# Optimization experiments

Measured on AMD Instinct MI355X. Metric: run time of the kernel, lower is better.

The kernel has to match this reference:

```python
import math
import jax, jax.numpy as jnp
import numpy as np

B, T, D = 8, 2048, 512
EPS = 1e-5


def _gate(x, W, b, a, g, beta):
    # Linear -> PReLU (single shared slope a) -> LayerNorm -> sigmoid
    h = x @ W.T + b
    h = jnp.where(h >= 0, h, a * h)
    mu = jnp.mean(h, axis=-1, keepdims=True)
    var = jnp.var(h, axis=-1, keepdims=True)
    h = (h - mu) / jnp.sqrt(var + EPS) * g + beta
    return jax.nn.sigmoid(h)


def setup_inputs() -> dict:
    key = jax.random.key(0)
    ks = jax.random.split(key, 12)
    lin = lambda k: jax.random.normal(k, (D, D), jnp.float32) * 0.02
    z = jnp.zeros((D,), jnp.float32)
    o = jnp.ones((D,), jnp.float32)
    a0 = jnp.float32(0.25)  # PReLU default init
    inp = {
        "query": jax.random.normal(ks[0], (B, T, D), jnp.float32),
        "value": jax.random.normal(ks[1], (B, T, D), jnp.float32),
        "aux_emb": jax.random.normal(ks[2], (B, 1, D), jnp.float32),
        # ragged valid lengths in [T//2, T] to keep every sample realistic
        "input_len": jax.random.randint(ks[3], (B,), T // 2, T + 1),
        "Wq": lin(ks[4]), "bq": z,
        "Wqg": lin(ks[5]), "bqg": z, "aq": a0, "gq": o, "betaq": z,
        "Wkg": lin(ks[6]), "bkg": z, "ak": a0, "gk": o, "betak": z,
        "Wvg": lin(ks[7]), "bvg": z, "av": a0, "gv": o, "betav": z,
        "Wsig": lin(ks[8]), "bsig": z,
        "Wtan": lin(ks[9]), "btan": z,
    }
    return inp


def reference(query, value, aux_emb, input_len,
              Wq, bq,
              Wqg, bqg, aq, gq, betaq,
              Wkg, bkg, ak, gk, betak,
              Wvg, bvg, av, gv, betav,
              Wsig, bsig, Wtan, btan):
    q = query @ Wq.T + bq
    q = q * _gate(aux_emb, Wqg, bqg, aq, gq, betaq)          # [B,T,D]
    k = value * _gate(aux_emb, Wkg, bkg, ak, gk, betak)      # [B,T,D]
    vg = _gate(aux_emb, Wvg, bvg, av, gv, betav)             # [B,1,D]
    vg = jax.nn.sigmoid(vg @ Wsig.T + bsig) * jnp.tanh(vg @ Wtan.T + btan)
    v = value * vg                                           # [B,T,D]

    w = jnp.einsum('btd,bsd->bts', q, k) / math.sqrt(D)      # [B,T,T]
    r = jnp.arange(T)
    causal = (r[:, None] >= r[None, :]).astype(w.dtype)      # tril ones
    w = w * causal
    w = jnp.where(w == 0.0, -jnp.inf, w)  # torch quirk: exact zeros -> -inf
    L = input_len[:, None, None]                              # [B,1,1]
    invalid = (r[None, :, None] < L) & (r[None, None, :] >= L)
    w = jnp.where(invalid, -jnp.inf, w)
    p = jax.nn.softmax(w, axis=-1)
    # rows beyond input_len are padding: zero them (torch code produced NaN
    # there via -inf*0; intended semantics is zeroed padding rows)
    row_valid = (r[None, :, None] < L).astype(p.dtype)        # [B,T,1]
    p = p * row_valid
    return p @ v                                              # [B,T,D]
```

## Files before the change

kernel.cpp:

```cpp
#include <hip/hip_runtime.h>
#include <hip/hip_bf16.h>
#include <stdint.h>

#define BB 8
#define TT 2048
#define DD 512

typedef __attribute__((ext_vector_type(8))) __bf16 bf16x8;
typedef __attribute__((ext_vector_type(4))) float f32x4;

__device__ __forceinline__ unsigned short f2bf(float f) {
    unsigned u = __builtin_bit_cast(unsigned, f);
    unsigned r = u + 0x7fffu + ((u >> 16) & 1u);
    return (unsigned short)(r >> 16);
}

__device__ __forceinline__ void gload_lds16(const unsigned short* g, unsigned short* l) {
    __builtin_amdgcn_global_load_lds(
        (const __attribute__((address_space(1))) void*)g,
        (__attribute__((address_space(3))) void*)l, 16, 0, 0);
}

__global__ __launch_bounds__(256) void gates_mv1(
    const float* __restrict__ aux,
    const float* __restrict__ Wqg, const float* __restrict__ bqg, const float* __restrict__ aq,
    const float* __restrict__ Wkg, const float* __restrict__ bkg, const float* __restrict__ ak,
    const float* __restrict__ Wvg, const float* __restrict__ bvg, const float* __restrict__ av,
    float* __restrict__ h) {
    __shared__ float saux[BB * DD];
    int tid = threadIdx.x;
#pragma unroll
    for (int i = 0; i < 4; i++) {
        int idx = tid + i * 256;
        ((float4*)saux)[idx] = ((const float4*)aux)[idx];
    }
    __syncthreads();
    int wave = (blockIdx.x * 256 + tid) >> 6;
    int lane = tid & 63;
    int g = wave >> 9, r = wave & 511;
    const float* W    = (g == 0) ? Wqg : (g == 1) ? Wkg : Wvg;
    const float* bias = (g == 0) ? bqg : (g == 1) ? bkg : bvg;
    const float* alpha = (g == 0) ? aq : (g == 1) ? ak : av;
    const float4* Wrow = (const float4*)(W + (size_t)r * DD);
    float acc[BB];
#pragma unroll
    for (int b = 0; b < BB; b++) acc[b] = 0.f;
#pragma unroll
    for (int c = 0; c < 2; c++) {
        float4 w4 = Wrow[lane + c * 64];
#pragma unroll
        for (int b = 0; b < BB; b++) {
            float4 a4 = ((const float4*)(saux + b * DD))[lane + c * 64];
            acc[b] += w4.x * a4.x + w4.y * a4.y + w4.z * a4.z + w4.w * a4.w;
        }
    }
#pragma unroll
    for (int b = 0; b < BB; b++) {
#pragma unroll
        for (int s = 1; s < 64; s <<= 1) acc[b] += __shfl_xor(acc[b], s, 64);
    }
    if (lane == 0) {
        float bi = bias[r], a = alpha[0];
#pragma unroll
        for (int b = 0; b < BB; b++) {
            float v = acc[b] + bi;
            v = (v >= 0.f) ? v : a * v;
            h[(g * BB + b) * DD + r] = v;
        }
    }
}

__global__ __launch_bounds__(512) void gates_norm(
    const float* __restrict__ h,
    const float* __restrict__ gq, const float* __restrict__ betaq,
    const float* __restrict__ gk, const float* __restrict__ betak,
    const float* __restrict__ gv, const float* __restrict__ betav,
    float* __restrict__ qgate, float* __restrict__ kgate, float* __restrict__ vg) {
    int g = blockIdx.x >> 3, b = blockIdx.x & 7, tid = threadIdx.x;
    __shared__ float red[DD], red2[DD];
    float hv = h[(g * BB + b) * DD + tid];
    red[tid] = hv; red2[tid] = hv * hv;
    __syncthreads();
    for (int s = 256; s > 0; s >>= 1) {
        if (tid < s) { red[tid] += red[tid + s]; red2[tid] += red2[tid + s]; }
        __syncthreads();
    }
    float mu = red[0] * (1.f / DD);
    float var = red2[0] * (1.f / DD) - mu * mu;
    const float* gg = (g == 0) ? gq : (g == 1) ? gk : gv;
    const float* be = (g == 0) ? betaq : (g == 1) ? betak : betav;
    float val = (hv - mu) * rsqrtf(var + 1e-5f) * gg[tid] + be[tid];
    float sg = 1.f / (1.f + expf(-val));
    float* outp = (g == 0) ? qgate : (g == 1) ? kgate : vg;
    outp[b * DD + tid] = sg;
}

__global__ __launch_bounds__(256) void gates_mv2(
    const float* __restrict__ vg,
    const float* __restrict__ Wsig, const float* __restrict__ bsig,
    const float* __restrict__ Wtan, const float* __restrict__ btan,
    float* __restrict__ vgate) {
    __shared__ float svg[BB * DD];
    int tid = threadIdx.x;
#pragma unroll
    for (int i = 0; i < 4; i++) {
        int idx = tid + i * 256;
        ((float4*)svg)[idx] = ((const float4*)vg)[idx];
    }
    __syncthreads();
    int r = (blockIdx.x * 256 + tid) >> 6;
    int lane = tid & 63;
    const float4* Ws = (const float4*)(Wsig + (size_t)r * DD);
    const float4* Wt = (const float4*)(Wtan + (size_t)r * DD);
    float as_[BB], at_[BB];
#pragma unroll
    for (int b = 0; b < BB; b++) { as_[b] = 0.f; at_[b] = 0.f; }
#pragma unroll
    for (int c = 0; c < 2; c++) {
        float4 w1 = Ws[lane + c * 64];
        float4 w2 = Wt[lane + c * 64];
#pragma unroll
        for (int b = 0; b < BB; b++) {
            float4 a4 = ((const float4*)(svg + b * DD))[lane + c * 64];
            as_[b] += w1.x * a4.x + w1.y * a4.y + w1.z * a4.z + w1.w * a4.w;
            at_[b] += w2.x * a4.x + w2.y * a4.y + w2.z * a4.z + w2.w * a4.w;
        }
    }
#pragma unroll
    for (int b = 0; b < BB; b++) {
#pragma unroll
        for (int s = 1; s < 64; s <<= 1) {
            as_[b] += __shfl_xor(as_[b], s, 64);
            at_[b] += __shfl_xor(at_[b], s, 64);
        }
    }
    if (lane == 0) {
        float b1 = bsig[r], b2 = btan[r];
#pragma unroll
        for (int b = 0; b < BB; b++) {
            float s1 = 1.f / (1.f + expf(-(as_[b] + b1)));
            float s2 = tanhf(at_[b] + b2);
            vgate[b * DD + r] = s1 * s2;
        }
    }
}

__global__ __launch_bounds__(256) void convert_kernel(
    const float* __restrict__ query, const float* __restrict__ Wq,
    const float* __restrict__ value,
    const float* __restrict__ kgate, const float* __restrict__ vgate,
    unsigned short* __restrict__ queryb, unsigned short* __restrict__ Wqb,
    unsigned short* __restrict__ kb, unsigned short* __restrict__ vbT) {
    __shared__ float tile[32][33];
    int bi = blockIdx.x, tid = threadIdx.x;
    if (bi < 8192) {
        int idx = bi * 256 + tid;
        float4 q4 = ((const float4*)query)[idx];
        ushort4 oq;
        oq.x = f2bf(q4.x); oq.y = f2bf(q4.y); oq.z = f2bf(q4.z); oq.w = f2bf(q4.w);
        ((ushort4*)queryb)[idx] = oq;
    } else if (bi < 8448) {
        int idx = (bi - 8192) * 256 + tid;
        float4 w4 = ((const float4*)Wq)[idx];
        ushort4 o;
        o.x = f2bf(w4.x); o.y = f2bf(w4.y); o.z = f2bf(w4.z); o.w = f2bf(w4.w);
        ((ushort4*)Wqb)[idx] = o;
    } else {
        int vb = bi - 8448;
        int tIdx = vb & 63, dIdx = (vb >> 6) & 15, b = vb >> 10;
        int t0 = tIdx * 32, d0 = dIdx * 32;
        int tx = tid & 31, ty = tid >> 5;
        float kg = kgate[b * DD + d0 + tx];
#pragma unroll
        for (int i = 0; i < 4; i++) {
            int t = t0 + ty + i * 8;
            float v = value[((size_t)b * TT + t) * DD + d0 + tx];
            tile[ty + i * 8][tx] = v;
            kb[((size_t)b * TT + t) * DD + d0 + tx] = f2bf(v * kg);
        }
        __syncthreads();
#pragma unroll
        for (int i = 0; i < 4; i++) {
            int d = d0 + ty + i * 8;
            float g = vgate[b * DD + d];
            vbT[((size_t)b * DD + d) * TT + t0 + tx] = f2bf(tile[tx][ty + i * 8] * g);
        }
    }
}

#define STAGE_AB(BUF, K0)                                                                 \
    _Pragma("unroll") for (int i = 0; i < 2; i++) {                                       \
        int idx = tid * 8 + i * 2048;                                                     \
        int r = idx >> 5;                                                                 \
        int cg = ((idx >> 3) & 3) ^ ((r >> 1) & 3);                                       \
        gload_lds16(&Ap_[(size_t)r * lda_ + (K0) + cg * 8], &As[BUF][idx]);               \
        gload_lds16(&Bp_[(size_t)r * ldb_ + (K0) + cg * 8], &Bs[BUF][idx]);               \
    }

#define GEMM_CORE(APTR, ALDA, BPTR, BLDA, KSTART, KEND)                                   \
    __shared__ __align__(16) unsigned short As[2][128 * 32];                              \
    __shared__ __align__(16) unsigned short Bs[2][128 * 32];                              \
    const unsigned short* Ap_ = (APTR);                                                   \
    const unsigned short* Bp_ = (BPTR);                                                   \
    const int lda_ = (ALDA), ldb_ = (BLDA);                                               \
    int tid = threadIdx.x;                                                                \
    int lane = tid & 63, wid = tid >> 6;                                                  \
    int wm = (wid >> 1) * 64, wn = (wid & 1) * 64;                                        \
    int lm = lane & 15, quad = lane >> 4;                                                 \
    f32x4 acc[4][4];                                                                      \
    _Pragma("unroll") for (int im = 0; im < 4; im++)                                      \
        _Pragma("unroll") for (int in = 0; in < 4; in++)                                  \
            acc[im][in] = (f32x4){0.f, 0.f, 0.f, 0.f};                                    \
    STAGE_AB(0, (KSTART))                                                                 \
    int cur_ = 0;                                                                         \
    for (int k0 = (KSTART); k0 < (KEND); k0 += 32) {                                      \
        __syncthreads();                                                                  \
        if (k0 + 32 < (KEND)) { STAGE_AB(cur_ ^ 1, k0 + 32) }                             \
        bf16x8 af[4], bf_[4];                                                             \
        _Pragma("unroll") for (int i = 0; i < 4; i++) {                                   \
            int row = wm + i * 16 + lm;                                                   \
            af[i] = *(const bf16x8*)&As[cur_][row * 32 + (quad ^ ((row >> 1) & 3)) * 8];  \
        }                                                                                 \
        _Pragma("unroll") for (int i = 0; i < 4; i++) {                                   \
            int row = wn + i * 16 + lm;                                                   \
            bf_[i] = *(const bf16x8*)&Bs[cur_][row * 32 + (quad ^ ((row >> 1) & 3)) * 8]; \
        }                                                                                 \
        _Pragma("unroll") for (int im = 0; im < 4; im++)                                  \
            _Pragma("unroll") for (int in = 0; in < 4; in++)                              \
                acc[im][in] = __builtin_amdgcn_mfma_f32_16x16x32_bf16(af[im], bf_[in],    \
                                                                     acc[im][in], 0, 0, 0);\
        cur_ ^= 1;                                                                        \
    }

__global__ __launch_bounds__(256) void qgemm_kernel(
    const unsigned short* __restrict__ Amat, const unsigned short* __restrict__ Bmat,
    const float* __restrict__ bq, const float* __restrict__ qgate,
    unsigned short* __restrict__ qb) {
    int m0 = blockIdx.x * 128, n0 = blockIdx.y * 128;
    const unsigned short* Ap = Amat + (size_t)m0 * DD;
    const unsigned short* Bp = Bmat + (size_t)n0 * DD;
    GEMM_CORE(Ap, DD, Bp, DD, 0, DD)
    int b = m0 >> 11;
#pragma unroll
    for (int im = 0; im < 4; im++) {
        int row = m0 + wm + im * 16 + quad * 4;
#pragma unroll
        for (int in = 0; in < 4; in++) {
            int col = n0 + wn + in * 16 + lm;
            float bias = bq[col];
            float g = qgate[b * DD + col];
#pragma unroll
            for (int r = 0; r < 4; r++) {
                float v = (acc[im][in][r] + bias) * g;
                qb[(size_t)(row + r) * DD + col] = f2bf(v);
            }
        }
    }
}

__global__ __launch_bounds__(256) void scores_kernel(
    const unsigned short* __restrict__ qb, const unsigned short* __restrict__ kb,
    unsigned short* __restrict__ P, float* __restrict__ rowsum) {
    int b = blockIdx.z;
    int idx = blockIdx.x;
    int mt = (int)((sqrtf(8.f * idx + 1.f) - 1.f) * 0.5f);
    while ((mt + 1) * (mt + 2) / 2 <= idx) mt++;
    while (mt * (mt + 1) / 2 > idx) mt--;
    int nt = idx - mt * (mt + 1) / 2;
    int t0 = mt * 128, s0 = nt * 128;
    const unsigned short* Ap = qb + ((size_t)b * TT + t0) * DD;
    const unsigned short* Bp = kb + ((size_t)b * TT + s0) * DD;
    GEMM_CORE(Ap, DD, Bp, DD, 0, DD)
    const float scale = 0.044194173824159216f;
    unsigned short* Ptile = P + ((size_t)b * 136 + (size_t)mt * (mt + 1) / 2 + nt) * 16384;
#pragma unroll
    for (int im = 0; im < 4; im++) {
        int ltb = wm + im * 16 + quad * 4;
        float rs[4] = {0.f, 0.f, 0.f, 0.f};
#pragma unroll
        for (int in = 0; in < 4; in++) {
            int ls = wn + in * 16 + lm;
            int s = s0 + ls;
#pragma unroll
            for (int r = 0; r < 4; r++) {
                float p = (s <= t0 + ltb + r) ? expf(acc[im][in][r] * scale) : 0.f;
                Ptile[(size_t)(ltb + r) * 128 + ls] = f2bf(p);
                rs[r] += p;
            }
        }
#pragma unroll
        for (int r = 0; r < 4; r++) {
            float v = rs[r];
            v += __shfl_xor(v, 1, 64);
            v += __shfl_xor(v, 2, 64);
            v += __shfl_xor(v, 4, 64);
            v += __shfl_xor(v, 8, 64);
            if (lm == 0) atomicAdd(&rowsum[b * TT + t0 + ltb + r], v);
        }
    }
}

__global__ __launch_bounds__(256) void out_kernel(
    const unsigned short* __restrict__ P, const unsigned short* __restrict__ vbT,
    const float* __restrict__ rowsum, const int* __restrict__ input_len,
    float* __restrict__ out) {
    int nt = blockIdx.x;
    int pr = blockIdx.y;
    int b = blockIdx.z;
    int n0 = nt * 128;
    int L = input_len[b];

    __shared__ __align__(16) unsigned short As[2][64 * 64];
    __shared__ __align__(16) unsigned short Bs[2][128 * 64];
    int tid = threadIdx.x;
    int lane = tid & 63, wid = tid >> 6;
    int wm = (wid >> 1) * 32, wn = (wid & 1) * 64;
    int lm = lane & 15, quad = lane >> 4;

#pragma unroll
    for (int half = 0; half < 2; half++) {
        int mt = half ? (31 - pr) : pr;
        int t0 = mt * 64;
        int mt128 = mt >> 1;
        int rowoff = (mt & 1) * 64;
        size_t triBase = ((size_t)b * 136 + (size_t)mt128 * (mt128 + 1) / 2) * 16384;
        int ksteps = mt + 1;

        f32x4 acc[2][4];
#pragma unroll
        for (int im = 0; im < 2; im++)
#pragma unroll
            for (int in = 0; in < 4; in++) acc[im][in] = (f32x4){0.f, 0.f, 0.f, 0.f};

#define OUT_STAGE(BUF, KS)                                                              \
        {                                                                               \
            int k0s = (KS) * 64;                                                        \
            int stile = k0s >> 7;                                                       \
            int coloff = k0s & 64;                                                      \
            _Pragma("unroll") for (int i = 0; i < 2; i++) {                             \
                int idx = tid * 8 + i * 2048;                                           \
                int r = idx >> 6;                                                       \
                int c = (idx >> 3) & 7;                                                 \
                int cs = c ^ (r & 7);                                                   \
                const unsigned short* ag = P + triBase + (size_t)stile * 16384 +        \
                                           (size_t)(rowoff + r) * 128 + coloff + cs * 8;\
                gload_lds16(ag, &As[BUF][idx]);                                         \
            }                                                                           \
            _Pragma("unroll") for (int i = 0; i < 4; i++) {                             \
                int idx = tid * 8 + i * 2048;                                           \
                int r = idx >> 6;                                                       \
                int c = (idx >> 3) & 7;                                                 \
                int cs = c ^ (r & 7);                                                   \
                gload_lds16(&vbT[(size_t)(b * DD + n0 + r) * TT + k0s + cs * 8],        \
                            &Bs[BUF][idx]);                                             \
            }                                                                           \
        }

        OUT_STAGE(0, 0)
        int cur = 0;
        for (int ks = 0; ks < ksteps; ks++) {
            __syncthreads();
            if (ks + 1 < ksteps) { OUT_STAGE(cur ^ 1, ks + 1) }
            bf16x8 af[2][2], bf_[4][2];
#pragma unroll
            for (int kk = 0; kk < 2; kk++) {
#pragma unroll
                for (int i = 0; i < 2; i++) {
                    int row = wm + i * 16 + lm;
                    af[i][kk] = *(const bf16x8*)&As[cur][row * 64 + ((kk * 4 + quad) ^ (row & 7)) * 8];
                }
#pragma unroll
                for (int i = 0; i < 4; i++) {
                    int row = wn + i * 16 + lm;
                    bf_[i][kk] = *(const bf16x8*)&Bs[cur][row * 64 + ((kk * 4 + quad) ^ (row & 7)) * 8];
                }
            }
#pragma unroll
            for (int kk = 0; kk < 2; kk++)
#pragma unroll
                for (int im = 0; im < 2; im++)
#pragma unroll
                    for (int in = 0; in < 4; in++)
                        acc[im][in] = __builtin_amdgcn_mfma_f32_16x16x32_bf16(
                            af[im][kk], bf_[in][kk], acc[im][in], 0, 0, 0);
            cur ^= 1;
        }
        __syncthreads();
#undef OUT_STAGE

#pragma unroll
        for (int im = 0; im < 2; im++) {
            int tbase = t0 + wm + im * 16 + quad * 4;
#pragma unroll
            for (int r = 0; r < 4; r++) {
                int t = tbase + r;
                float inv = 1.f / rowsum[b * TT + t];
                bool valid = (t < L);
#pragma unroll
                for (int in = 0; in < 4; in++) {
                    int n = n0 + wn + in * 16 + lm;
                    float o = valid ? acc[im][in][r] * inv : 0.f;
                    out[((size_t)b * TT + t) * DD + n] = o;
                }
            }
        }
    }
}

extern "C" void kernel_launch(void* const* d_in, const int* in_sizes, int n_in,
                              void* d_out, int out_size, void* d_ws, size_t ws_size,
                              hipStream_t stream) {
    const float* query = (const float*)d_in[0];
    const float* value = (const float*)d_in[1];
    const float* aux   = (const float*)d_in[2];
    const int*   ilen  = (const int*)d_in[3];
    const float* Wq    = (const float*)d_in[4];
    const float* bq    = (const float*)d_in[5];
    const float* Wqg   = (const float*)d_in[6];
    const float* bqg   = (const float*)d_in[7];
    const float* aq    = (const float*)d_in[8];
    const float* gq    = (const float*)d_in[9];
    const float* betaq = (const float*)d_in[10];
    const float* Wkg   = (const float*)d_in[11];
    const float* bkg   = (const float*)d_in[12];
    const float* ak    = (const float*)d_in[13];
    const float* gk    = (const float*)d_in[14];
    const float* betak = (const float*)d_in[15];
    const float* Wvg   = (const float*)d_in[16];
    const float* bvg   = (const float*)d_in[17];
    const float* av    = (const float*)d_in[18];
    const float* gv    = (const float*)d_in[19];
    const float* betav = (const float*)d_in[20];
    const float* Wsig  = (const float*)d_in[21];
    const float* bsig  = (const float*)d_in[22];
    const float* Wtan  = (const float*)d_in[23];
    const float* btan  = (const float*)d_in[24];

    char* ws = (char*)d_ws;
    float* qgate          = (float*)(ws + 0);
    float* kgate          = (float*)(ws + 16384);
    float* vgate          = (float*)(ws + 32768);
    float* rowsum         = (float*)(ws + 49152);
    unsigned short* Wqb   = (unsigned short*)(ws + 114688);
    unsigned short* queryb= (unsigned short*)(ws + 638976);
    unsigned short* qb    = (unsigned short*)(ws + 17416192);
    unsigned short* kb    = (unsigned short*)(ws + 34193408);
    unsigned short* vbT   = (unsigned short*)(ws + 50970624);
    unsigned short* P     = (unsigned short*)(ws + 67747840);
    float* hbuf           = (float*)(ws + 67747840);
    float* vg             = (float*)(ws + 67747840 + 49152);

    hipMemsetAsync(rowsum, 0, BB * TT * sizeof(float), stream);

    gates_mv1<<<384, 256, 0, stream>>>(aux, Wqg, bqg, aq, Wkg, bkg, ak, Wvg, bvg, av, hbuf);
    gates_norm<<<24, 512, 0, stream>>>(hbuf, gq, betaq, gk, betak, gv, betav,
                                       qgate, kgate, vg);
    gates_mv2<<<128, 256, 0, stream>>>(vg, Wsig, bsig, Wtan, btan, vgate);

    convert_kernel<<<16640, 256, 0, stream>>>(query, Wq, value, kgate, vgate,
                                              queryb, Wqb, kb, vbT);
    qgemm_kernel<<<dim3((BB * TT) / 128, DD / 128), 256, 0, stream>>>(queryb, Wqb, bq, qgate, qb);
    scores_kernel<<<dim3(136, 1, BB), 256, 0, stream>>>(qb, kb, P, rowsum);
    out_kernel<<<dim3(4, 16, BB), 256, 0, stream>>>(P, vbT, rowsum, ilen, (float*)d_out);
}
```

Before: 273.2 us.

## Fuse scores and PV into one flash-style attention kernel without materialized P

Replaces the separate scores kernel (which wrote bf16 exp-scores to a global P buffer plus atomic rowsums) and the output GEMM kernel with a single attention kernel. Each 512-thread block processes two paired 32-row query strips, keeping Q in LDS, streaming K and V tiles through a shared double buffer, writing P only to LDS and accumulating row sums locally. This removes the global P round trip, the rowsum memset and one kernel launch. In exchange there are only 256 blocks, each with small 32-row tiles and many barriers, and K/V are re-read once per strip, so occupancy and reuse may be lower.

```diff
diff --git a/kernel.cpp b/kernel.cpp
--- a/kernel.cpp
+++ b/kernel.cpp
@@ -258,153 +258,187 @@
     }
 }
 
-__global__ __launch_bounds__(256) void scores_kernel(
+__global__ __launch_bounds__(512) void attn_kernel(
     const unsigned short* __restrict__ qb, const unsigned short* __restrict__ kb,
-    unsigned short* __restrict__ P, float* __restrict__ rowsum) {
-    int b = blockIdx.z;
-    int idx = blockIdx.x;
-    int mt = (int)((sqrtf(8.f * idx + 1.f) - 1.f) * 0.5f);
-    while ((mt + 1) * (mt + 2) / 2 <= idx) mt++;
-    while (mt * (mt + 1) / 2 > idx) mt--;
-    int nt = idx - mt * (mt + 1) / 2;
-    int t0 = mt * 128, s0 = nt * 128;
-    const unsigned short* Ap = qb + ((size_t)b * TT + t0) * DD;
-    const unsigned short* Bp = kb + ((size_t)b * TT + s0) * DD;
-    GEMM_CORE(Ap, DD, Bp, DD, 0, DD)
+    const unsigned short* __restrict__ vbT, const int* __restrict__ input_len,
+    float* __restrict__ out) {
+    int bid = blockIdx.x;
+    int p = bid >> 3, b = bid & 7;
+    int L = input_len[b];
+    int tid = threadIdx.x;
+    int lane = tid & 63, w = tid >> 6;
+    int lm = lane & 15, quad = lane >> 4;
+    const size_t bTT = (size_t)b * TT;
     const float scale = 0.044194173824159216f;
-    unsigned short* Ptile = P + ((size_t)b * 136 + (size_t)mt * (mt + 1) / 2 + nt) * 16384;
-#pragma unroll
-    for (int im = 0; im < 4; im++) {
-        int ltb = wm + im * 16 + quad * 4;
-        float rs[4] = {0.f, 0.f, 0.f, 0.f};
-#pragma unroll
-        for (int in = 0; in < 4; in++) {
-            int ls = wn + in * 16 + lm;
-            int s = s0 + ls;
+
+    __shared__ __align__(16) unsigned short Qs[32 * 512];
+    __shared__ __align__(16) unsigned short KV[2][2048 * 8];
+    __shared__ __align__(16) unsigned short Ps[32 * 256];
+    __shared__ float rs_lds[32];
+
+#define STAGE_K(DST, KV0, D0)                                                     \
+    _Pragma("unroll") for (int i_ = 0; i_ < 4; i_++) {                            \
+        int idx_ = tid + i_ * 512;                                                \
+        int r_ = idx_ >> 3, c_ = idx_ & 7;                                        \
+        int g_ = c_ ^ (r_ & 7);                                                   \
+        gload_lds16(&kb[(bTT + (KV0) + r_) * DD + (D0) + g_ * 8],                 \
+                    &KV[DST][idx_ * 8]);                                          \
+    }
+#define STAGE_V(DST, KVC)                                                         \
+    _Pragma("unroll") for (int i_ = 0; i_ < 4; i_++) {                            \
+        int idx_ = tid + i_ * 512;                                                \
+        int r_ = idx_ >> 2, c_ = idx_ & 3;                                        \
+        int g_ = c_ ^ (r_ & 3);                                                   \
+        gload_lds16(&vbT[((size_t)(b * DD) + r_) * TT + (KVC) + g_ * 8],          \
+                    &KV[DST][idx_ * 8]);                                          \
+    }
+
+#pragma unroll 1
+    for (int half = 0; half < 2; half++) {
+        int strip = half ? (63 - p) : p;
+        int t0 = strip * 32;
+        int nk = (strip >> 3) + 1;
+
+        __syncthreads();
+#pragma unroll
+        for (int i_ = 0; i_ < 4; i_++) {
+            int idx_ = tid + i_ * 512;
+            int r_ = idx_ >> 6, c_ = idx_ & 63;
+            int gc_ = (c_ & 56) | ((c_ ^ r_) & 7);
+            gload_lds16(&qb[(bTT + t0 + r_) * DD + gc_ * 8], &Qs[idx_ * 8]);
+        }
+        STAGE_K(0, 0, 0)
+        int buf = 0;
+
+        f32x4 oacc[2][4];
+#pragma unroll
+        for (int mi = 0; mi < 2; mi++)
+#pragma unroll
+            for (int ni = 0; ni < 4; ni++) oacc[mi][ni] = (f32x4){0.f, 0.f, 0.f, 0.f};
+        float rsum[2][4];
+#pragma unroll
+        for (int mi = 0; mi < 2; mi++)
+#pragma unroll
+            for (int r = 0; r < 4; r++) rsum[mi][r] = 0.f;
+
+        for (int m = 0; m < nk; m++) {
+            int kv0 = m * 256;
+            f32x4 sacc[2][2];
+#pragma unroll
+            for (int mi = 0; mi < 2; mi++)
+#pragma unroll
+                for (int ni = 0; ni < 2; ni++) sacc[mi][ni] = (f32x4){0.f, 0.f, 0.f, 0.f};
+
+#pragma unroll 1
+            for (int ds = 0; ds < 8; ds++) {
+                __syncthreads();
+                if (ds < 7) { STAGE_K(buf ^ 1, kv0, (ds + 1) * 64) }
+                else        { STAGE_V(buf ^ 1, kv0) }
+#pragma unroll
+                for (int kk = 0; kk < 2; kk++) {
+                    bf16x8 aq[2], bk[2];
+#pragma unroll
+                    for (int mi = 0; mi < 2; mi++) {
+                        int row = mi * 16 + lm;
+                        int c = ds * 8 + kk * 4 + quad;
+                        int sc = (c & 56) | ((c ^ row) & 7);
+                        aq[mi] = *(const bf16x8*)&Qs[(row << 9) + sc * 8];
+                    }
+#pragma unroll
+                    for (int ni = 0; ni < 2; ni++) {
+                        int row = w * 32 + ni * 16 + lm;
+                        int sc = (kk * 4 + quad) ^ (row & 7);
+                        bk[ni] = *(const bf16x8*)&KV[buf][(row << 6) + sc * 8];
+                    }
+#pragma unroll
+                    for (int mi = 0; mi < 2; mi++)
+#pragma unroll
+                        for (int ni = 0; ni < 2; ni++)
+                            sacc[mi][ni] = __builtin_amdgcn_mfma_f32_16x16x32_bf16(
+                                aq[mi], bk[ni], sacc[mi][ni], 0, 0, 0);
+                }
+                buf ^= 1;
+            }
+
+#pragma unroll
+            for (int mi = 0; mi < 2; mi++)
+#pragma unroll
+                for (int ni = 0; ni < 2; ni++)
+#pragma unroll
+                    for (int r = 0; r < 4; r++) {
+                        int trow = mi * 16 + quad * 4 + r;
+                        int t = t0 + trow;
+                        int e = w * 32 + ni * 16 + lm;
+                        int s = kv0 + e;
+                        float pv = (s <= t) ? expf(sacc[mi][ni][r] * scale) : 0.f;
+                        rsum[mi][r] += pv;
+                        int c = e >> 3, o = e & 7;
+                        int sc = (c & 24) | ((c ^ trow) & 7);
+                        Ps[trow * 256 + sc * 8 + o] = f2bf(pv);
+                    }
+
+#pragma unroll 1
+            for (int kc = 0; kc < 8; kc++) {
+                __syncthreads();
+                if (kc < 7)           { STAGE_V(buf ^ 1, kv0 + (kc + 1) * 32) }
+                else if (m + 1 < nk)  { STAGE_K(buf ^ 1, kv0 + 256, 0) }
+                bf16x8 pa[2], vb[4];
+#pragma unroll
+                for (int mi = 0; mi < 2; mi++) {
+                    int row = mi * 16 + lm;
+                    int c = kc * 4 + quad;
+                    int sc = (c & 24) | ((c ^ row) & 7);
+                    pa[mi] = *(const bf16x8*)&Ps[row * 256 + sc * 8];
+                }
+#pragma unroll
+                for (int ni = 0; ni < 4; ni++) {
+                    int row = w * 64 + ni * 16 + lm;
+                    int sc = quad ^ (row & 3);
+                    vb[ni] = *(const bf16x8*)&KV[buf][(row << 5) + sc * 8];
+                }
+#pragma unroll
+                for (int mi = 0; mi < 2; mi++)
+#pragma unroll
+                    for (int ni = 0; ni < 4; ni++)
+                        oacc[mi][ni] = __builtin_amdgcn_mfma_f32_16x16x32_bf16(
+                            pa[mi], vb[ni], oacc[mi][ni], 0, 0, 0);
+                buf ^= 1;
+            }
+        }
+
+        __syncthreads();
+        if (tid < 32) rs_lds[tid] = 0.f;
+        __syncthreads();
+#pragma unroll
+        for (int mi = 0; mi < 2; mi++)
 #pragma unroll
             for (int r = 0; r < 4; r++) {
-                float p = (s <= t0 + ltb + r) ? expf(acc[im][in][r] * scale) : 0.f;
-                Ptile[(size_t)(ltb + r) * 128 + ls] = f2bf(p);
-                rs[r] += p;
+                float v = rsum[mi][r];
+                v += __shfl_xor(v, 1, 64);
+                v += __shfl_xor(v, 2, 64);
+                v += __shfl_xor(v, 4, 64);
+                v += __shfl_xor(v, 8, 64);
+                if (lm == 0) atomicAdd(&rs_lds[mi * 16 + quad * 4 + r], v);
             }
-        }
-#pragma unroll
-        for (int r = 0; r < 4; r++) {
-            float v = rs[r];
-            v += __shfl_xor(v, 1, 64);
-            v += __shfl_xor(v, 2, 64);
-            v += __shfl_xor(v, 4, 64);
-            v += __shfl_xor(v, 8, 64);
-            if (lm == 0) atomicAdd(&rowsum[b * TT + t0 + ltb + r], v);
-        }
-    }
-}
-
-__global__ __launch_bounds__(256) void out_kernel(
-    const unsigned short* __restrict__ P, const unsigned short* __restrict__ vbT,
-    const float* __restrict__ rowsum, const int* __restrict__ input_len,
-    float* __restrict__ out) {
-    int nt = blockIdx.x;
-    int pr = blockIdx.y;
-    int b = blockIdx.z;
-    int n0 = nt * 128;
-    int L = input_len[b];
-
-    __shared__ __align__(16) unsigned short As[2][64 * 64];
-    __shared__ __align__(16) unsigned short Bs[2][128 * 64];
-    int tid = threadIdx.x;
-    int lane = tid & 63, wid = tid >> 6;
-    int wm = (wid >> 1) * 32, wn = (wid & 1) * 64;
-    int lm = lane & 15, quad = lane >> 4;
-
-#pragma unroll
-    for (int half = 0; half < 2; half++) {
-        int mt = half ? (31 - pr) : pr;
-        int t0 = mt * 64;
-        int mt128 = mt >> 1;
-        int rowoff = (mt & 1) * 64;
-        size_t triBase = ((size_t)b * 136 + (size_t)mt128 * (mt128 + 1) / 2) * 16384;
-        int ksteps = mt + 1;
-
-        f32x4 acc[2][4];
-#pragma unroll
-        for (int im = 0; im < 2; im++)
-#pragma unroll
-            for (int in = 0; in < 4; in++) acc[im][in] = (f32x4){0.f, 0.f, 0.f, 0.f};
-
-#define OUT_STAGE(BUF, KS)                                                              \
-        {                                                                               \
-            int k0s = (KS) * 64;                                                        \
-            int stile = k0s >> 7;                                                       \
-            int coloff = k0s & 64;                                                      \
-            _Pragma("unroll") for (int i = 0; i < 2; i++) {                             \
-                int idx = tid * 8 + i * 2048;                                           \
-                int r = idx >> 6;                                                       \
-                int c = (idx >> 3) & 7;                                                 \
-                int cs = c ^ (r & 7);                                                   \
-                const unsigned short* ag = P + triBase + (size_t)stile * 16384 +        \
-                                           (size_t)(rowoff + r) * 128 + coloff + cs * 8;\
-                gload_lds16(ag, &As[BUF][idx]);                                         \
-            }                                                                           \
-            _Pragma("unroll") for (int i = 0; i < 4; i++) {                             \
-                int idx = tid * 8 + i * 2048;                                           \
-                int r = idx >> 6;                                                       \
-                int c = (idx >> 3) & 7;                                                 \
-                int cs = c ^ (r & 7);                                                   \
-                gload_lds16(&vbT[(size_t)(b * DD + n0 + r) * TT + k0s + cs * 8],        \
-                            &Bs[BUF][idx]);                                             \
-            }                                                                           \
-        }
-
-        OUT_STAGE(0, 0)
-        int cur = 0;
-        for (int ks = 0; ks < ksteps; ks++) {
-            __syncthreads();
-            if (ks + 1 < ksteps) { OUT_STAGE(cur ^ 1, ks + 1) }
-            bf16x8 af[2][2], bf_[4][2];
-#pragma unroll
-            for (int kk = 0; kk < 2; kk++) {
-#pragma unroll
-                for (int i = 0; i < 2; i++) {
-                    int row = wm + i * 16 + lm;
-                    af[i][kk] = *(const bf16x8*)&As[cur][row * 64 + ((kk * 4 + quad) ^ (row & 7)) * 8];
-                }
-#pragma unroll
-                for (int i = 0; i < 4; i++) {
-                    int row = wn + i * 16 + lm;
-                    bf_[i][kk] = *(const bf16x8*)&Bs[cur][row * 64 + ((kk * 4 + quad) ^ (row & 7)) * 8];
+        __syncthreads();
+#pragma unroll
+        for (int mi = 0; mi < 2; mi++)
+#pragma unroll
+            for (int r = 0; r < 4; r++) {
+                int trow = mi * 16 + quad * 4 + r;
+                int t = t0 + trow;
+                float inv = 1.f / rs_lds[trow];
+                bool valid = (t < L);
+#pragma unroll
+                for (int ni = 0; ni < 4; ni++) {
+                    int n = w * 64 + ni * 16 + lm;
+                    float o = valid ? oacc[mi][ni][r] * inv : 0.f;
+                    out[(bTT + t) * DD + n] = o;
                 }
             }
-#pragma unroll
-            for (int kk = 0; kk < 2; kk++)
-#pragma unroll
-                for (int im = 0; im < 2; im++)
-#pragma unroll
-                    for (int in = 0; in < 4; in++)
-                        acc[im][in] = __builtin_amdgcn_mfma_f32_16x16x32_bf16(
-                            af[im][kk], bf_[in][kk], acc[im][in], 0, 0, 0);
-            cur ^= 1;
-        }
-        __syncthreads();
-#undef OUT_STAGE
-
-#pragma unroll
-        for (int im = 0; im < 2; im++) {
-            int tbase = t0 + wm + im * 16 + quad * 4;
-#pragma unroll
-            for (int r = 0; r < 4; r++) {
-                int t = tbase + r;
-                float inv = 1.f / rowsum[b * TT + t];
-                bool valid = (t < L);
-#pragma unroll
-                for (int in = 0; in < 4; in++) {
-                    int n = n0 + wn + in * 16 + lm;
-                    float o = valid ? acc[im][in][r] * inv : 0.f;
-                    out[((size_t)b * TT + t) * DD + n] = o;
-                }
-            }
-        }
-    }
+    }
+#undef STAGE_K
+#undef STAGE_V
 }
 
 extern "C" void kernel_launch(void* const* d_in, const int* in_sizes, int n_in,
@@ -440,17 +474,13 @@
     float* qgate          = (float*)(ws + 0);
     float* kgate          = (float*)(ws + 16384);
     float* vgate          = (float*)(ws + 32768);
-    float* rowsum         = (float*)(ws + 49152);
     unsigned short* Wqb   = (unsigned short*)(ws + 114688);
     unsigned short* queryb= (unsigned short*)(ws + 638976);
     unsigned short* qb    = (unsigned short*)(ws + 17416192);
     unsigned short* kb    = (unsigned short*)(ws + 34193408);
     unsigned short* vbT   = (unsigned short*)(ws + 50970624);
-    unsigned short* P     = (unsigned short*)(ws + 67747840);
     float* hbuf           = (float*)(ws + 67747840);
     float* vg             = (float*)(ws + 67747840 + 49152);
-
-    hipMemsetAsync(rowsum, 0, BB * TT * sizeof(float), stream);
 
     gates_mv1<<<384, 256, 0, stream>>>(aux, Wqg, bqg, aq, Wkg, bkg, ak, Wvg, bvg, av, hbuf);
     gates_norm<<<24, 512, 0, stream>>>(hbuf, gq, betaq, gk, betak, gv, betav,
@@ -460,6 +490,5 @@
     convert_kernel<<<16640, 256, 0, stream>>>(query, Wq, value, kgate, vgate,
                                               queryb, Wqb, kb, vbT);
     qgemm_kernel<<<dim3((BB * TT) / 128, DD / 128), 256, 0, stream>>>(queryb, Wqb, bq, qgate, qb);
-    scores_kernel<<<dim3(136, 1, BB), 256, 0, stream>>>(qb, kb, P, rowsum);
-    out_kernel<<<dim3(4, 16, BB), 256, 0, stream>>>(P, vbT, rowsum, ilen, (float*)d_out);
-}
+    attn_kernel<<<256, 512, 0, stream>>>(qb, kb, vbT, ilen, (float*)d_out);
+}
```

Result: slower. 302.9 us (+10.9%).

## Vectorize value transpose/convert tiles and interleave batches across workgroup order

Applied to the files above, without the earlier changes.

The value conversion path moves from 32x32 tiles with scalar loads and stores to 64x64 tiles using float4 loads and 16-byte bf16 stores for both the gated key copy and the transposed value copy. This reduces the block count and the number of narrow memory transactions. The scores and output kernels also remap the block index so the batch index varies fastest, spreading each batch's work across the dispatch order. The transposed LDS read with a 65-float stride may still cause some bank conflicts.

```diff
diff --git a/kernel.cpp b/kernel.cpp
--- a/kernel.cpp
+++ b/kernel.cpp
@@ -8,6 +8,7 @@
 
 typedef __attribute__((ext_vector_type(8))) __bf16 bf16x8;
 typedef __attribute__((ext_vector_type(4))) float f32x4;
+typedef __attribute__((ext_vector_type(8))) unsigned short ushort8_t;
 
 __device__ __forceinline__ unsigned short f2bf(float f) {
     unsigned u = __builtin_bit_cast(unsigned, f);
@@ -151,7 +152,7 @@
     const float* __restrict__ kgate, const float* __restrict__ vgate,
     unsigned short* __restrict__ queryb, unsigned short* __restrict__ Wqb,
     unsigned short* __restrict__ kb, unsigned short* __restrict__ vbT) {
-    __shared__ float tile[32][33];
+    __shared__ float tileF[64][65];
     int bi = blockIdx.x, tid = threadIdx.x;
     if (bi < 8192) {
         int idx = bi * 256 + tid;
@@ -167,24 +168,42 @@
         ((ushort4*)Wqb)[idx] = o;
     } else {
         int vb = bi - 8448;
-        int tIdx = vb & 63, dIdx = (vb >> 6) & 15, b = vb >> 10;
-        int t0 = tIdx * 32, d0 = dIdx * 32;
-        int tx = tid & 31, ty = tid >> 5;
-        float kg = kgate[b * DD + d0 + tx];
-#pragma unroll
-        for (int i = 0; i < 4; i++) {
-            int t = t0 + ty + i * 8;
-            float v = value[((size_t)b * TT + t) * DD + d0 + tx];
-            tile[ty + i * 8][tx] = v;
-            kb[((size_t)b * TT + t) * DD + d0 + tx] = f2bf(v * kg);
-        }
+        int tIdx = vb & 31, dIdx = (vb >> 5) & 7, b = vb >> 8;
+        int t0 = tIdx * 64, d0 = dIdx * 64;
+        int row = tid >> 2;
+        int cg = tid & 3;
+        float v[16], kgv[16];
+        const float* src = &value[((size_t)b * TT + t0 + row) * DD + d0 + cg * 16];
+#pragma unroll
+        for (int j = 0; j < 4; j++) {
+            float4 f = ((const float4*)src)[j];
+            v[j * 4 + 0] = f.x; v[j * 4 + 1] = f.y; v[j * 4 + 2] = f.z; v[j * 4 + 3] = f.w;
+            float4 g = *(const float4*)&kgate[b * DD + d0 + cg * 16 + j * 4];
+            kgv[j * 4 + 0] = g.x; kgv[j * 4 + 1] = g.y; kgv[j * 4 + 2] = g.z; kgv[j * 4 + 3] = g.w;
+        }
+        ushort8_t kb8[2];
+#pragma unroll
+        for (int h = 0; h < 2; h++)
+#pragma unroll
+            for (int j = 0; j < 8; j++)
+                kb8[h][j] = f2bf(v[h * 8 + j] * kgv[h * 8 + j]);
+        unsigned short* kdst = &kb[((size_t)b * TT + t0 + row) * DD + d0 + cg * 16];
+        *(ushort8_t*)&kdst[0] = kb8[0];
+        *(ushort8_t*)&kdst[8] = kb8[1];
+#pragma unroll
+        for (int j = 0; j < 16; j++) tileF[row][cg * 16 + j] = v[j];
         __syncthreads();
-#pragma unroll
-        for (int i = 0; i < 4; i++) {
-            int d = d0 + ty + i * 8;
-            float g = vgate[b * DD + d];
-            vbT[((size_t)b * DD + d) * TT + t0 + tx] = f2bf(tile[tx][ty + i * 8] * g);
-        }
+        int d = row;
+        float g = vgate[b * DD + d0 + d];
+        ushort8_t o8[2];
+#pragma unroll
+        for (int h = 0; h < 2; h++)
+#pragma unroll
+            for (int j = 0; j < 8; j++)
+                o8[h][j] = f2bf(tileF[cg * 16 + h * 8 + j][d] * g);
+        unsigned short* vdst = &vbT[((size_t)b * DD + d0 + d) * TT + t0 + cg * 16];
+        *(ushort8_t*)&vdst[0] = o8[0];
+        *(ushort8_t*)&vdst[8] = o8[1];
     }
 }
 
@@ -261,8 +280,9 @@
 __global__ __launch_bounds__(256) void scores_kernel(
     const unsigned short* __restrict__ qb, const unsigned short* __restrict__ kb,
     unsigned short* __restrict__ P, float* __restrict__ rowsum) {
-    int b = blockIdx.z;
-    int idx = blockIdx.x;
+    int lin = blockIdx.x + 136 * blockIdx.z;
+    int b = lin & 7;
+    int idx = lin >> 3;
     int mt = (int)((sqrtf(8.f * idx + 1.f) - 1.f) * 0.5f);
     while ((mt + 1) * (mt + 2) / 2 <= idx) mt++;
     while (mt * (mt + 1) / 2 > idx) mt--;
@@ -304,9 +324,11 @@
     const unsigned short* __restrict__ P, const unsigned short* __restrict__ vbT,
     const float* __restrict__ rowsum, const int* __restrict__ input_len,
     float* __restrict__ out) {
-    int nt = blockIdx.x;
-    int pr = blockIdx.y;
-    int b = blockIdx.z;
+    int lin = blockIdx.x + 4 * blockIdx.y + 64 * blockIdx.z;
+    int b = lin & 7;
+    int rem = lin >> 3;
+    int nt = rem & 3;
+    int pr = rem >> 2;
     int n0 = nt * 128;
     int L = input_len[b];
 
@@ -457,7 +479,7 @@
                                        qgate, kgate, vg);
     gates_mv2<<<128, 256, 0, stream>>>(vg, Wsig, bsig, Wtan, btan, vgate);
 
-    convert_kernel<<<16640, 256, 0, stream>>>(query, Wq, value, kgate, vgate,
+    convert_kernel<<<10496, 256, 0, stream>>>(query, Wq, value, kgate, vgate,
                                               queryb, Wqb, kb, vbT);
     qgemm_kernel<<<dim3((BB * TT) / 128, DD / 128), 256, 0, stream>>>(queryb, Wqb, bq, qgate, qb);
     scores_kernel<<<dim3(136, 1, BB), 256, 0, stream>>>(qb, kb, P, rowsum);
```

Result: faster. 259.5 us (-5.0%).
